# Performance work log

Measured on AMD Instinct MI355X. Metric: run time of the kernel, lower is better.

## Reference

```python
import jax, jax.numpy as jnp
import numpy as np
import math

B, S, H, NH = 4, 1024, 1024, 16
HD = H // NH  # 64
MAX_REL = 127


def relative_position_encoding(depth, max_length, max_relative_position):
    vocab_size = max_relative_position * 2 + 1
    range_vec = np.arange(max_length)
    distance = range_vec[None, :] - range_vec[:, None]  # matches range_mat - range_mat.T
    final_mat = np.clip(distance, -max_relative_position, max_relative_position) + max_relative_position
    position = np.arange(vocab_size, dtype=np.float32)[:, None]
    div_term = np.exp(np.arange(0, depth, 2, dtype=np.float32) * (-math.log(10000.0) / depth))
    table = np.zeros((vocab_size, depth), dtype=np.float32)
    table[:, 0::2] = np.sin(position * div_term)
    table[:, 1::2] = np.cos(position * div_term)
    return jnp.asarray(table[final_mat])  # [max_length, max_length, depth]


def setup_inputs() -> dict:
    key = jax.random.key(0)
    ks = jax.random.split(key, 4)
    sc = 0.02
    return {
        "hidden_states": jax.random.normal(ks[0], (B, S, H), dtype=jnp.float32),
        "Wq": jax.random.normal(ks[1], (H, H), dtype=jnp.float32) * sc,
        "bq": jnp.zeros((H,), dtype=jnp.float32),
        "Wk": jax.random.normal(ks[2], (H, H), dtype=jnp.float32) * sc,
        "bk": jnp.zeros((H,), dtype=jnp.float32),
        "Wv": jax.random.normal(ks[3], (H, H), dtype=jnp.float32) * sc,
        "bv": jnp.zeros((H,), dtype=jnp.float32),
        "rel_pos": relative_position_encoding(HD, S, MAX_REL),  # [S, S, HD] sinusoidal buffer
    }


def reference(hidden_states, Wq, bq, Wk, bk, Wv, bv, rel_pos):
    b, s, h = hidden_states.shape

    def heads(x):  # [b,s,h] -> [b,nh,s,hd]
        return x.reshape(b, s, NH, HD).transpose(0, 2, 1, 3)

    q = heads(hidden_states @ Wq.T + bq)
    k = heads(hidden_states @ Wk.T + bk)
    v = heads(hidden_states @ Wv.T + bv)

    scores = jnp.einsum("bhqd,bhkd->bhqk", q, k)
    # query-relative-key positional term
    scores = scores + jnp.einsum("bhqd,qkd->bhqk", q, rel_pos)
    scores = scores / math.sqrt(HD)

    probs = jax.nn.softmax(scores, axis=-1)  # dropout p=0 (eval)

    ctx = jnp.einsum("bhqk,bhkd->bhqd", probs, v)
    # prob-relative-value positional term
    ctx = ctx + jnp.einsum("bhqk,qkd->bhqd", probs, rel_pos)

    return ctx.transpose(0, 2, 1, 3).reshape(b, s, h)
```

## Files before the change

### kernel.cpp

```cpp
#include <hip/hip_runtime.h>
#include <stdint.h>


typedef __bf16 bf16x8 __attribute__((ext_vector_type(8)));
typedef float f32x4 __attribute__((ext_vector_type(4)));
typedef uint16_t u16x8 __attribute__((ext_vector_type(8)));
typedef uint16_t u16x4 __attribute__((ext_vector_type(4)));

#define K2E 0.18033688011112042f

__device__ __forceinline__ float hw_exp2(float x) {
    return __builtin_amdgcn_exp2f(x);
}
__device__ __forceinline__ uint16_t f2bf(float f) {
    uint32_t u = __builtin_bit_cast(uint32_t, f);
    return (uint16_t)((u + 0x7FFFu + ((u >> 16) & 1u)) >> 16);
}
__device__ __forceinline__ uint16_t f2bf_rn(float f) {
    return __builtin_bit_cast(uint16_t, (__bf16)f);
}
__device__ __forceinline__ float bf2f(uint16_t h) {
    uint32_t u = ((uint32_t)h) << 16;
    return __builtin_bit_cast(float, u);
}
__device__ __forceinline__ f32x4 mfma16(bf16x8 a, bf16x8 b, f32x4 c) {
    return __builtin_amdgcn_mfma_f32_16x16x32_bf16(a, b, c, 0, 0, 0);
}
__device__ __forceinline__ bf16x8 ldg8(const uint16_t* p) {
    return __builtin_bit_cast(bf16x8, *(const u16x8*)p);
}
__device__ __forceinline__ bf16x8 lds8(const void* base, int byteoff) {
    return __builtin_bit_cast(bf16x8, *(const u16x8*)((const char*)base + byteoff));
}

__global__ void k_cast_all(const float* __restrict__ hs, const float* __restrict__ wq,
                           const float* __restrict__ wk, const float* __restrict__ wv,
                           const float* __restrict__ rel,
                           uint16_t* __restrict__ hs_bf, uint16_t* __restrict__ w_bf,
                           uint16_t* __restrict__ tab, uint16_t* __restrict__ tabT) {
    int b = blockIdx.x;
    if (b >= 3584) {
        int idx = (b - 3584) * 256 + threadIdx.x;
        int j = idx >> 6, d = idx & 63;
        float v = 0.0f;
        if (j < 255) v = rel[((size_t)512 * 1024 + (512 + j - 127)) * 64 + d];
        uint16_t h = f2bf(v);
        tab[j * 64 + d] = h;
        tabT[d * 256 + j] = h;
        return;
    }
    const float* src;
    uint16_t* dst;
    int i;
    if (b < 2048)      { src = hs; dst = hs_bf;           i = b * 256 + threadIdx.x; }
    else if (b < 2560) { src = wq; dst = w_bf;            i = (b - 2048) * 256 + threadIdx.x; }
    else if (b < 3072) { src = wk; dst = w_bf + 1048576;  i = (b - 2560) * 256 + threadIdx.x; }
    else               { src = wv; dst = w_bf + 2097152;  i = (b - 3072) * 256 + threadIdx.x; }
    float4 a = ((const float4*)src)[2 * i];
    float4 c = ((const float4*)src)[2 * i + 1];
    u16x8 o;
    o[0] = f2bf(a.x); o[1] = f2bf(a.y); o[2] = f2bf(a.z); o[3] = f2bf(a.w);
    o[4] = f2bf(c.x); o[5] = f2bf(c.y); o[6] = f2bf(c.z); o[7] = f2bf(c.w);
    ((u16x8*)dst)[i] = o;
}

__launch_bounds__(256)
__global__ void k_gemm_qkv3(const uint16_t* __restrict__ A, const uint16_t* __restrict__ Wt,
                            const float* __restrict__ bq, const float* __restrict__ bk,
                            const float* __restrict__ bvp, uint16_t* __restrict__ qout,
                            uint16_t* __restrict__ kout, uint16_t* __restrict__ vt) {
    __shared__ uint16_t Sh[2 * 128 * 64];
    uint16_t* As = Sh;
    uint16_t* Bs = Sh + 8192;
    int bid = blockIdx.x;
    int xcd = bid & 7, idx = bid >> 3;
    int m0 = (xcd * 4 + (idx & 3)) * 128;
    int n0 = (idx >> 2) * 128;
    int tid = threadIdx.x;
    int w = tid >> 6, l = tid & 63, lg = l >> 4, ln = l & 15;
    int wm = w >> 1, wn = w & 1;
    int lrow = tid >> 3, lcol = (tid & 7) * 8;
    f32x4 acc[4][4] = {};
    for (int kt = 0; kt < 16; ++kt) {
        int k0 = kt * 64;
        __syncthreads();
#pragma unroll
        for (int c = 0; c < 4; ++c) {
            int row = c * 32 + lrow;
            __builtin_amdgcn_global_load_lds(
                (const __attribute__((address_space(1))) void*)(A + (size_t)(m0 + row) * 1024 + k0 + lcol),
                (__attribute__((address_space(3))) void*)&As[row * 64 + lcol], 16, 0, 0);
            __builtin_amdgcn_global_load_lds(
                (const __attribute__((address_space(1))) void*)(Wt + (size_t)(n0 + row) * 1024 + k0 + lcol),
                (__attribute__((address_space(3))) void*)&Bs[row * 64 + lcol], 16, 0, 0);
        }
        __syncthreads();
#pragma unroll
        for (int ks = 0; ks < 2; ++ks) {
            bf16x8 af[4], bfr[4];
#pragma unroll
            for (int mi = 0; mi < 4; ++mi)
                af[mi] = ldg8(&As[(wm * 64 + mi * 16 + ln) * 64 + ks * 32 + lg * 8]);
#pragma unroll
            for (int ni = 0; ni < 4; ++ni)
                bfr[ni] = ldg8(&Bs[(wn * 64 + ni * 16 + ln) * 64 + ks * 32 + lg * 8]);
#pragma unroll
            for (int mi = 0; mi < 4; ++mi)
#pragma unroll
                for (int ni = 0; ni < 4; ++ni)
                    acc[mi][ni] = mfma16(af[mi], bfr[ni], acc[mi][ni]);
        }
    }
    int b = m0 >> 10, s0r = m0 & 1023;
    int which = n0 >> 10, nbase = n0 & 1023;
    __syncthreads();
    if (which < 2) {
        uint16_t* qk = which == 0 ? qout : kout;
        const float* bp = which == 0 ? bq : bk;
#pragma unroll
        for (int ni = 0; ni < 4; ++ni) {
            int d2 = wn * 64 + ni * 16 + ln;
            float bb = bp[nbase + d2];
#pragma unroll
            for (int mi = 0; mi < 4; ++mi)
#pragma unroll
                for (int r = 0; r < 4; ++r) {
                    int s2 = wm * 64 + mi * 16 + lg * 4 + r;
                    *(uint16_t*)((char*)Sh + ((s2 * 256 + d2 * 2) ^ (((s2 >> 2) & 7) << 4))) =
                        f2bf(acc[mi][ni][r] + bb);
                }
        }
        __syncthreads();
#pragma unroll
        for (int hh = 0; hh < 2; ++hh) {
            int h = (nbase >> 6) + hh;
#pragma unroll
            for (int i = 0; i < 4; ++i) {
                int s2 = i * 32 + w * 8 + (l >> 3);
                int d2 = hh * 64 + (l & 7) * 8;
                u16x8 vv = *(u16x8*)((char*)Sh + ((s2 * 256 + d2 * 2) ^ (((s2 >> 2) & 7) << 4)));
                *(u16x8*)&qk[(((size_t)(b * 16 + h)) * 1024 + s0r + s2) * 64 + (d2 & 63)] = vv;
            }
        }
    } else {
#pragma unroll
        for (int ni = 0; ni < 4; ++ni) {
            int d2 = wn * 64 + ni * 16 + ln;
            float bb = bvp[nbase + d2];
#pragma unroll
            for (int mi = 0; mi < 4; ++mi) {
                int s2 = wm * 64 + mi * 16 + lg * 4;
                u16x4 pv;
#pragma unroll
                for (int r = 0; r < 4; ++r) pv[r] = f2bf(acc[mi][ni][r] + bb);
                *(u16x4*)((char*)Sh + ((d2 * 256 + s2 * 2) ^ ((d2 & 7) << 4))) = pv;
            }
        }
        __syncthreads();
#pragma unroll
        for (int i = 0; i < 8; ++i) {
            int d2 = i * 16 + w * 4 + (l >> 4);
            int s2 = (l & 15) * 8;
            u16x8 vv = *(u16x8*)((char*)Sh + ((d2 * 256 + s2 * 2) ^ ((d2 & 7) << 4)));
            int nr = nbase + d2;
            int h = nr >> 6, d = nr & 63;
            *(u16x8*)&vt[(((size_t)(b * 16 + h)) * 64 + d) * 1024 + s0r + s2] = vv;
        }
    }
}

__launch_bounds__(256)
__global__ void k_r_gemm(const uint16_t* __restrict__ q, const uint16_t* __restrict__ tab,
                         uint16_t* __restrict__ R) {
    __shared__ uint16_t Qs[64 * 72];
    int m0 = blockIdx.x * 64;
    int tid = threadIdx.x;
    int w = tid >> 6, l = tid & 63, lg = l >> 4, ln = l & 15;
#pragma unroll
    for (int c = 0; c < 2; ++c) {
        int idx = c * 256 + tid; int row = idx >> 3, seg = idx & 7;
        *(u16x8*)&Qs[row * 72 + seg * 8] =
            *(const u16x8*)(q + (size_t)(m0 + row) * 64 + seg * 8);
    }
    __syncthreads();
    bf16x8 aq[4][2];
#pragma unroll
    for (int mi = 0; mi < 4; ++mi)
#pragma unroll
        for (int ks = 0; ks < 2; ++ks)
            aq[mi][ks] = ldg8(&Qs[(mi * 16 + ln) * 72 + ks * 32 + lg * 8]);
    f32x4 acc[4][4] = {};
#pragma unroll
    for (int ni = 0; ni < 4; ++ni) {
        int j = w * 64 + ni * 16 + ln;
#pragma unroll
        for (int ks = 0; ks < 2; ++ks) {
            bf16x8 bt = ldg8(tab + j * 64 + ks * 32 + lg * 8);
#pragma unroll
            for (int mi = 0; mi < 4; ++mi)
                acc[mi][ni] = mfma16(aq[mi][ks], bt, acc[mi][ni]);
        }
    }
#pragma unroll
    for (int ni = 0; ni < 4; ++ni)
#pragma unroll
        for (int mi = 0; mi < 4; ++mi)
#pragma unroll
            for (int r = 0; r < 4; ++r)
                R[(size_t)(m0 + mi * 16 + lg * 4 + r) * 256 + w * 64 + ni * 16 + ln] =
                    f2bf(acc[mi][ni][r]);
}

__device__ __forceinline__ void softmax_grp(
    const f32x4 (&acc)[4], int kt, int qbase, int ln, const uint16_t* __restrict__ Rrow,
    float rel_lo2, float rel_hi2, uint16_t* prow, int lg,
    float& lloc, float& slo, float& shi, uint32_t (&pk)[4][2]) {
    int cls = (kt * 64 - (qbase + 15) >= 127) ? 2
            : ((kt * 64 + 63 - qbase <= -127) ? 0 : 1);
    int qg = qbase + ln;
    float sv[16];
    if (cls == 2) {
#pragma unroll
        for (int m = 0; m < 4; ++m)
#pragma unroll
            for (int r = 0; r < 4; ++r) sv[m * 4 + r] = fmaf(acc[m][r], K2E, rel_hi2);
    } else if (cls == 0) {
#pragma unroll
        for (int m = 0; m < 4; ++m)
#pragma unroll
            for (int r = 0; r < 4; ++r) sv[m * 4 + r] = fmaf(acc[m][r], K2E, rel_lo2);
    } else {
#pragma unroll
        for (int m = 0; m < 4; ++m) {
            int base = kt * 64 + (m >> 1) * 32 + lg * 8 + (m & 1) * 4 - qg;
#pragma unroll
            for (int r = 0; r < 4; ++r) {
                int dj = base + r;
                int djc = dj < -127 ? -127 : (dj > 127 ? 127 : dj);
                float rel = bf2f(Rrow[djc + 127]);
                sv[m * 4 + r] = (acc[m][r] + rel) * K2E;
            }
        }
    }
    float pm[4];
    if (cls == 1) {
#pragma unroll
        for (int m = 0; m < 4; ++m) {
            int base = kt * 64 + (m >> 1) * 32 + lg * 8 + (m & 1) * 4 - qg;
            uint32_t w0 = 0, w1 = 0;
            float ps = 0.f;
#pragma unroll
            for (int r = 0; r < 4; ++r) {
                float P = hw_exp2(sv[m * 4 + r]);
                ps += P;
                uint32_t h = f2bf_rn(P);
                int dj = base + r;
                if (dj <= -127) slo += P;
                else if (dj >= 127) shi += P;
                else prow[dj + 127] = (uint16_t)h;
                if (r < 2) w0 |= h << (16 * r); else w1 |= h << (16 * (r - 2));
            }
            pm[m] = ps;
            pk[m][0] = w0; pk[m][1] = w1;
        }
    } else {
#pragma unroll
        for (int m = 0; m < 4; ++m) {
            uint32_t w0 = 0, w1 = 0;
            float ps = 0.f;
#pragma unroll
            for (int r = 0; r < 4; ++r) {
                float P = hw_exp2(sv[m * 4 + r]);
                ps += P;
                uint32_t h = f2bf_rn(P);
                if (r < 2) w0 |= h << (16 * r); else w1 |= h << (16 * (r - 2));
            }
            pm[m] = ps;
            pk[m][0] = w0; pk[m][1] = w1;
        }
        float ts = (pm[0] + pm[1]) + (pm[2] + pm[3]);
        if (cls == 2) shi += ts; else slo += ts;
    }
    lloc += (pm[0] + pm[1]) + (pm[2] + pm[3]);
}

__launch_bounds__(256, 2)
__global__ void k_attn_fused(const uint16_t* __restrict__ qb, const uint16_t* __restrict__ kb,
                             const uint16_t* __restrict__ vtb, const uint16_t* __restrict__ Rb,
                             const uint16_t* __restrict__ tabT, float* __restrict__ out) {
    __shared__ uint16_t Pagg[128 * 256];
    __shared__ uint16_t Kb[64 * 64];
    __shared__ uint16_t Vb[64 * 64];
    int bid = blockIdx.x;
    bid = (bid & 7) * 64 + (bid >> 3);
    int bh = bid >> 3, q0 = (bid & 7) * 128;
    int tid = threadIdx.x;
    int w = tid >> 6, l = tid & 63, lg = l >> 4, ln = l & 15;
    int qbaseA = q0 + w * 16, qbaseB = qbaseA + 64;
    int qA = qbaseA + ln, qB = qA + 64;
    bf16x8 qfA[2], qfB[2];
    {
        const uint16_t* qr = qb + ((size_t)bh * 1024 + qA) * 64;
        qfA[0] = ldg8(qr + lg * 8); qfA[1] = ldg8(qr + 32 + lg * 8);
        qr += 64 * 64;
        qfB[0] = ldg8(qr + lg * 8); qfB[1] = ldg8(qr + 32 + lg * 8);
    }
    const uint16_t* RrowA = Rb + ((size_t)bh * 1024 + qA) * 256;
    const uint16_t* RrowB = RrowA + 64 * 256;
    uint16_t* prowA = &Pagg[(w * 16 + ln) * 256];
    uint16_t* prowB = &Pagg[(64 + w * 16 + ln) * 256];
    {
        u16x8* pa = (u16x8*)&Pagg[(w * 16) * 256];
        u16x8* pb2 = (u16x8*)&Pagg[(64 + w * 16) * 256];
#pragma unroll
        for (int i = 0; i < 8; ++i) { pa[i * 64 + l] = (u16x8)0; pb2[i * 64 + l] = (u16x8)0; }
    }
    float relA_lo = bf2f(RrowA[0]) * K2E, relA_hi = bf2f(RrowA[254]) * K2E;
    float relB_lo = bf2f(RrowB[0]) * K2E, relB_hi = bf2f(RrowB[254]) * K2E;
    const int r0 = tid >> 3, c16 = tid & 7;
    const int r1 = 32 + r0;
    const int slotK0 = (r0 & 3) | ((r0 >> 1) & 4), slotK1 = (r1 & 3) | ((r1 >> 1) & 4);
    const int waK0 = (r0 * 128 + c16 * 16) ^ (slotK0 << 4);
    const int waK1 = (r1 * 128 + c16 * 16) ^ (slotK1 << 4);
    const int waV0 = (r0 * 128 + c16 * 16) ^ ((r0 & 7) << 4);
    const int waV1 = (r1 * 128 + c16 * 16) ^ ((r1 & 7) << 4);
    const uint16_t* kt_base = kb + ((size_t)bh * 1024) * 64;
    const uint16_t* vt_base = vtb + (size_t)bh * 64 * 1024;
    u16x8 kc0 = *(const u16x8*)(kt_base + (size_t)r0 * 64 + c16 * 8);
    u16x8 kc1 = *(const u16x8*)(kt_base + (size_t)r1 * 64 + c16 * 8);
    u16x8 vc0 = *(const u16x8*)(vt_base + (size_t)r0 * 1024 + c16 * 8);
    u16x8 vc1 = *(const u16x8*)(vt_base + (size_t)r1 * 1024 + c16 * 8);
    float llocA = 0.f, sloA = 0.f, shiA = 0.f;
    float llocB = 0.f, sloB = 0.f, shiB = 0.f;
    f32x4 oaccA[4] = {}, oaccB[4] = {};
    for (int kt = 0; kt < 16; ++kt) {
        __syncthreads();
        *(u16x8*)((char*)Kb + waK0) = kc0;
        *(u16x8*)((char*)Kb + waK1) = kc1;
        *(u16x8*)((char*)Vb + waV0) = vc0;
        *(u16x8*)((char*)Vb + waV1) = vc1;
        __syncthreads();
        if (kt < 15) {
            const uint16_t* kn = kt_base + (size_t)(kt + 1) * 64 * 64;
            const uint16_t* vn = vt_base + (kt + 1) * 64;
            kc0 = *(const u16x8*)(kn + (size_t)r0 * 64 + c16 * 8);
            kc1 = *(const u16x8*)(kn + (size_t)r1 * 64 + c16 * 8);
            vc0 = *(const u16x8*)(vn + (size_t)r0 * 1024 + c16 * 8);
            vc1 = *(const u16x8*)(vn + (size_t)r1 * 1024 + c16 * 8);
        }
        f32x4 accA[4] = {}, accB[4] = {};
        __builtin_amdgcn_s_setprio(1);
#pragma unroll
        for (int m = 0; m < 4; ++m) {
            int rowp = ((m >> 1) << 5) + ((ln >> 2) << 3) + ((m & 1) << 2) + (ln & 3);
            bf16x8 a0 = lds8(Kb, (rowp * 128 + lg * 16) ^ ((ln & 7) << 4));
            bf16x8 a1 = lds8(Kb, (rowp * 128 + 64 + lg * 16) ^ ((ln & 7) << 4));
            accA[m] = mfma16(a0, qfA[0], accA[m]);
            accA[m] = mfma16(a1, qfA[1], accA[m]);
            accB[m] = mfma16(a0, qfB[0], accB[m]);
            accB[m] = mfma16(a1, qfB[1], accB[m]);
        }
        __builtin_amdgcn_s_setprio(0);
        uint32_t pkA[4][2], pkB[4][2];
        softmax_grp(accA, kt, qbaseA, ln, RrowA, relA_lo, relA_hi, prowA, lg,
                    llocA, sloA, shiA, pkA);
        softmax_grp(accB, kt, qbaseB, ln, RrowB, relB_lo, relB_hi, prowB, lg,
                    llocB, sloB, shiB, pkB);
        __builtin_amdgcn_s_setprio(1);
#pragma unroll
        for (int ks = 0; ks < 2; ++ks) {
            uint32_t fa[4] = {pkA[2 * ks][0], pkA[2 * ks][1], pkA[2 * ks + 1][0], pkA[2 * ks + 1][1]};
            uint32_t fb[4] = {pkB[2 * ks][0], pkB[2 * ks][1], pkB[2 * ks + 1][0], pkB[2 * ks + 1][1]};
            bf16x8 apA = __builtin_bit_cast(bf16x8, fa);
            bf16x8 apB = __builtin_bit_cast(bf16x8, fb);
#pragma unroll
            for (int nt = 0; nt < 4; ++nt) {
                int row = nt * 16 + ln;
                bf16x8 bv = lds8(Vb, (row * 128 + (ks * 4 + lg) * 16) ^ ((ln & 7) << 4));
                oaccA[nt] = mfma16(apA, bv, oaccA[nt]);
                oaccB[nt] = mfma16(apB, bv, oaccB[nt]);
            }
        }
        __builtin_amdgcn_s_setprio(0);
    }
    llocA += __shfl_xor(llocA, 16); llocA += __shfl_xor(llocA, 32);
    sloA  += __shfl_xor(sloA, 16);  sloA  += __shfl_xor(sloA, 32);
    shiA  += __shfl_xor(shiA, 16);  shiA  += __shfl_xor(shiA, 32);
    llocB += __shfl_xor(llocB, 16); llocB += __shfl_xor(llocB, 32);
    sloB  += __shfl_xor(sloB, 16);  sloB  += __shfl_xor(sloB, 32);
    shiB  += __shfl_xor(shiB, 16);  shiB  += __shfl_xor(shiB, 32);
    if (lg == 0) {
        prowA[0] = f2bf(sloA); prowA[254] = f2bf(shiA);
        prowB[0] = f2bf(sloB); prowB[254] = f2bf(shiB);
    }
#pragma unroll
    for (int ks8 = 0; ks8 < 8; ++ks8) {
        bf16x8 apA = ldg8(&Pagg[(w * 16 + ln) * 256 + ks8 * 32 + lg * 8]);
        bf16x8 apB = ldg8(&Pagg[(64 + w * 16 + ln) * 256 + ks8 * 32 + lg * 8]);
#pragma unroll
        for (int nt = 0; nt < 4; ++nt) {
            bf16x8 bt = ldg8(tabT + (size_t)(nt * 16 + ln) * 256 + ks8 * 32 + lg * 8);
            oaccA[nt] = mfma16(apA, bt, oaccA[nt]);
            oaccB[nt] = mfma16(apB, bt, oaccB[nt]);
        }
    }
    float rinvA[4], rinvB[4];
#pragma unroll
    for (int r = 0; r < 4; ++r) {
        rinvA[r] = 1.0f / __shfl(llocA, lg * 4 + r);
        rinvB[r] = 1.0f / __shfl(llocB, lg * 4 + r);
    }
    int b = bh >> 4, h = bh & 15;
#pragma unroll
    for (int nt = 0; nt < 4; ++nt) {
#pragma unroll
        for (int r = 0; r < 4; ++r) {
            int qoA = q0 + w * 16 + lg * 4 + r;
            out[((size_t)b * 1024 + qoA) * 1024 + h * 64 + nt * 16 + ln] = oaccA[nt][r] * rinvA[r];
            out[((size_t)b * 1024 + qoA + 64) * 1024 + h * 64 + nt * 16 + ln] = oaccB[nt][r] * rinvB[r];
        }
    }
}

extern "C" void kernel_launch(void* const* d_in, const int* in_sizes, int n_in,
                              void* d_out, int out_size, void* d_ws, size_t ws_size,
                              hipStream_t stream) {
    const float* hs  = (const float*)d_in[0];
    const float* Wq  = (const float*)d_in[1];
    const float* bq  = (const float*)d_in[2];
    const float* Wk  = (const float*)d_in[3];
    const float* bk  = (const float*)d_in[4];
    const float* Wv  = (const float*)d_in[5];
    const float* bv  = (const float*)d_in[6];
    const float* rel = (const float*)d_in[7];
    float* out = (float*)d_out;
    char* ws = (char*)d_ws;

    uint16_t* hs_bf = (uint16_t*)(ws);
    uint16_t* W_bf  = (uint16_t*)(ws + 8388608);
    uint16_t* q_bf  = (uint16_t*)(ws + 14680064);
    uint16_t* k_bf  = (uint16_t*)(ws + 23068672);
    uint16_t* vt_bf = (uint16_t*)(ws + 31457280);
    uint16_t* R_bf  = (uint16_t*)(ws + 48234496);
    uint16_t* tab   = (uint16_t*)(ws + 81788928);
    uint16_t* tabT  = (uint16_t*)(ws + 81821696);

    k_cast_all<<<3648, 256, 0, stream>>>(hs, Wq, Wk, Wv, rel, hs_bf, W_bf, tab, tabT);

    k_gemm_qkv3<<<768, 256, 0, stream>>>(hs_bf, W_bf, bq, bk, bv, q_bf, k_bf, vt_bf);
    k_r_gemm<<<1024, 256, 0, stream>>>(q_bf, tab, R_bf);

    k_attn_fused<<<512, 256, 0, stream>>>(q_bf, k_bf, vt_bf, R_bf, tabT, out);
}
```

Baseline: 129.0 us.

## Fuse relative-position R GEMM into attention kernel prologue

Removes the separate k_r_gemm launch. Each attention block now computes its own rows of R = q·table^T with MFMA, using the query fragments it already holds in registers, and writes them to the global R buffer. It then waits on vmcnt before reading R back per row. This saves one kernel launch and a pass of q reads, but adds a serialized prologue to the attention kernel and relies on same-wave global write/read ordering.

```diff
diff --git a/kernel.cpp b/kernel.cpp
--- a/kernel.cpp
+++ b/kernel.cpp
@@ -169,48 +169,6 @@
     }
 }
 
-__launch_bounds__(256)
-__global__ void k_r_gemm(const uint16_t* __restrict__ q, const uint16_t* __restrict__ tab,
-                         uint16_t* __restrict__ R) {
-    __shared__ uint16_t Qs[64 * 72];
-    int m0 = blockIdx.x * 64;
-    int tid = threadIdx.x;
-    int w = tid >> 6, l = tid & 63, lg = l >> 4, ln = l & 15;
-#pragma unroll
-    for (int c = 0; c < 2; ++c) {
-        int idx = c * 256 + tid; int row = idx >> 3, seg = idx & 7;
-        *(u16x8*)&Qs[row * 72 + seg * 8] =
-            *(const u16x8*)(q + (size_t)(m0 + row) * 64 + seg * 8);
-    }
-    __syncthreads();
-    bf16x8 aq[4][2];
-#pragma unroll
-    for (int mi = 0; mi < 4; ++mi)
-#pragma unroll
-        for (int ks = 0; ks < 2; ++ks)
-            aq[mi][ks] = ldg8(&Qs[(mi * 16 + ln) * 72 + ks * 32 + lg * 8]);
-    f32x4 acc[4][4] = {};
-#pragma unroll
-    for (int ni = 0; ni < 4; ++ni) {
-        int j = w * 64 + ni * 16 + ln;
-#pragma unroll
-        for (int ks = 0; ks < 2; ++ks) {
-            bf16x8 bt = ldg8(tab + j * 64 + ks * 32 + lg * 8);
-#pragma unroll
-            for (int mi = 0; mi < 4; ++mi)
-                acc[mi][ni] = mfma16(aq[mi][ks], bt, acc[mi][ni]);
-        }
-    }
-#pragma unroll
-    for (int ni = 0; ni < 4; ++ni)
-#pragma unroll
-        for (int mi = 0; mi < 4; ++mi)
-#pragma unroll
-            for (int r = 0; r < 4; ++r)
-                R[(size_t)(m0 + mi * 16 + lg * 4 + r) * 256 + w * 64 + ni * 16 + ln] =
-                    f2bf(acc[mi][ni][r]);
-}
-
 __device__ __forceinline__ void softmax_grp(
     const f32x4 (&acc)[4], int kt, int qbase, int ln, const uint16_t* __restrict__ Rrow,
     float rel_lo2, float rel_hi2, uint16_t* prow, int lg,
@@ -286,7 +244,8 @@
 
 __launch_bounds__(256, 2)
 __global__ void k_attn_fused(const uint16_t* __restrict__ qb, const uint16_t* __restrict__ kb,
-                             const uint16_t* __restrict__ vtb, const uint16_t* __restrict__ Rb,
+                             const uint16_t* __restrict__ vtb, uint16_t* Rb,
+                             const uint16_t* __restrict__ tab,
                              const uint16_t* __restrict__ tabT, float* __restrict__ out) {
     __shared__ uint16_t Pagg[128 * 256];
     __shared__ uint16_t Kb[64 * 64];
@@ -305,16 +264,31 @@
         qr += 64 * 64;
         qfB[0] = ldg8(qr + lg * 8); qfB[1] = ldg8(qr + 32 + lg * 8);
     }
+    {
+        u16x8* pa = (u16x8*)&Pagg[(w * 16) * 256];
+        u16x8* pb2 = (u16x8*)&Pagg[(64 + w * 16) * 256];
+#pragma unroll
+        for (int i = 0; i < 8; ++i) { pa[i * 64 + l] = (u16x8)0; pb2[i * 64 + l] = (u16x8)0; }
+    }
+    uint16_t* RoutA = Rb + ((size_t)bh * 1024 + qbaseA) * 256;
+#pragma unroll
+    for (int jt = 0; jt < 16; ++jt) {
+        bf16x8 bt0 = ldg8(tab + (size_t)(jt * 16 + ln) * 64 + lg * 8);
+        bf16x8 bt1 = ldg8(tab + (size_t)(jt * 16 + ln) * 64 + 32 + lg * 8);
+        f32x4 ra = {}, rb2 = {};
+        ra = mfma16(qfA[0], bt0, ra);  ra = mfma16(qfA[1], bt1, ra);
+        rb2 = mfma16(qfB[0], bt0, rb2); rb2 = mfma16(qfB[1], bt1, rb2);
+#pragma unroll
+        for (int r = 0; r < 4; ++r) {
+            RoutA[(size_t)(lg * 4 + r) * 256 + jt * 16 + ln] = f2bf(ra[r]);
+            RoutA[(size_t)(64 + lg * 4 + r) * 256 + jt * 16 + ln] = f2bf(rb2[r]);
+        }
+    }
+    asm volatile("s_waitcnt vmcnt(0)" ::: "memory");
     const uint16_t* RrowA = Rb + ((size_t)bh * 1024 + qA) * 256;
     const uint16_t* RrowB = RrowA + 64 * 256;
     uint16_t* prowA = &Pagg[(w * 16 + ln) * 256];
     uint16_t* prowB = &Pagg[(64 + w * 16 + ln) * 256];
-    {
-        u16x8* pa = (u16x8*)&Pagg[(w * 16) * 256];
-        u16x8* pb2 = (u16x8*)&Pagg[(64 + w * 16) * 256];
-#pragma unroll
-        for (int i = 0; i < 8; ++i) { pa[i * 64 + l] = (u16x8)0; pb2[i * 64 + l] = (u16x8)0; }
-    }
     float relA_lo = bf2f(RrowA[0]) * K2E, relA_hi = bf2f(RrowA[254]) * K2E;
     float relB_lo = bf2f(RrowB[0]) * K2E, relB_hi = bf2f(RrowB[254]) * K2E;
     const int r0 = tid >> 3, c16 = tid & 7;
@@ -448,7 +422,6 @@
     k_cast_all<<<3648, 256, 0, stream>>>(hs, Wq, Wk, Wv, rel, hs_bf, W_bf, tab, tabT);
 
     k_gemm_qkv3<<<768, 256, 0, stream>>>(hs_bf, W_bf, bq, bk, bv, q_bf, k_bf, vt_bf);
-    k_r_gemm<<<1024, 256, 0, stream>>>(q_bf, tab, R_bf);
-
-    k_attn_fused<<<512, 256, 0, stream>>>(q_bf, k_bf, vt_bf, R_bf, tabT, out);
-}
+
+    k_attn_fused<<<512, 256, 0, stream>>>(q_bf, k_bf, vt_bf, R_bf, tab, tabT, out);
+}
```

Result: faster. 126.2 us, median of 2 (-2.2%).
